# Kernel optimization log

Hardware: AMD Instinct MI355X
Metric: run time of the kernel (lower is better)

## Reference

```python
import jax, jax.numpy as jnp
import numpy as np

NUM_HEADS = 12


def setup_inputs() -> dict:
    key = jax.random.key(0)
    k1, k2, k3 = jax.random.split(key, 3)
    B, N, D = 8, 1024, 768
    x = jax.random.normal(k1, (B, N, D), dtype=jnp.float32)
    Wqkv = jax.random.normal(k2, (D, 3 * D), dtype=jnp.float32) * (D ** -0.5)
    Wproj = jax.random.normal(k3, (D, D), dtype=jnp.float32) * (D ** -0.5)
    bproj = jnp.zeros((D,), dtype=jnp.float32)
    return {"x": x, "Wqkv": Wqkv, "Wproj": Wproj, "bproj": bproj}


def reference(x, Wqkv, Wproj, bproj):
    B, N, D = x.shape
    H = NUM_HEADS
    d = D // H
    scale = d ** -0.5
    qkv = x @ Wqkv  # [B, N, 3D]; qkv_bias=False
    # 'b n (qkv h d) -> qkv b h n d'
    qkv = qkv.reshape(B, N, 3, H, d)
    q = jnp.transpose(qkv[:, :, 0], (0, 2, 1, 3))  # [B, H, N, d]
    k = jnp.transpose(qkv[:, :, 1], (0, 2, 1, 3))
    v = jnp.transpose(qkv[:, :, 2], (0, 2, 1, 3))
    attn = jnp.einsum('bhnd,bhmd->bhnm', q, k) * scale  # [B, H, N, N]
    attn = jax.nn.softmax(attn, axis=-1)
    out = jnp.einsum('bhnm,bhmd->bhnd', attn, v)  # [B, H, N, d]
    out = jnp.transpose(out, (0, 2, 1, 3)).reshape(B, N, D)  # 'b h n d -> b n (h d)'
    return out @ Wproj + bproj
```

## Files before the change

### kernel.cpp

```cpp
#include <hip/hip_runtime.h>
#include <math.h>
#include <stdint.h>

namespace {

constexpr int Nseq = 1024;
constexpr int Dm = 768;
constexpr int threeD = 2304;
constexpr int Mrows = 8192;
constexpr int Hh = 12;
constexpr float kScaleLog2 = 0.18033688011112042f;

using bf16x8 = __attribute__((ext_vector_type(8))) short;
using f32x4 = __attribute__((ext_vector_type(4))) float;
using f32x16 = __attribute__((ext_vector_type(16))) float;
using us4 = __attribute__((ext_vector_type(4))) unsigned short;

__device__ __forceinline__ unsigned short f2bf(float f) {
  union { float f; uint32_t u; } v;
  v.f = f;
  uint32_t r = v.u + 0x7fffu + ((v.u >> 16) & 1u);
  return (unsigned short)(r >> 16);
}

__device__ __forceinline__ float fexp2(float x) {
#if __has_builtin(__builtin_amdgcn_exp2f)
  return __builtin_amdgcn_exp2f(x);
#else
  float r;
  asm("v_exp_f32 %0, %1\n\ts_nop 0" : "=v"(r) : "v"(x));
  return r;
#endif
}

__device__ __forceinline__ uint32_t cvtpk_bf16(float lo, float hi) {
  uint32_t r;
  asm("v_cvt_pk_bf16_f32 %0, %1, %2" : "=v"(r) : "v"(lo), "v"(hi));
  return r;
}

__device__ __forceinline__ void gload_lds16(const void* g, void* l) {
  __builtin_amdgcn_global_load_lds(
      (const __attribute__((address_space(1))) unsigned int*)(uintptr_t)g,
      (__attribute__((address_space(3))) unsigned int*)(uintptr_t)l, 16, 0, 0);
}

__global__ __launch_bounds__(256) void cast_f32_bf16(
    const float* __restrict__ in, unsigned short* __restrict__ outp, int n4) {
  int i = blockIdx.x * blockDim.x + threadIdx.x;
  if (i < n4) {
    float4 v = ((const float4*)in)[i];
    us4 u = {f2bf(v.x), f2bf(v.y), f2bf(v.z), f2bf(v.w)};
    ((us4*)outp)[i] = u;
  }
}

__global__ __launch_bounds__(256) void transpose_cast(
    const float* __restrict__ W, unsigned short* __restrict__ Wt, int K, int N) {
  __shared__ unsigned short tile[32][33];
  const int n0 = blockIdx.x * 32, k0 = blockIdx.y * 32;
  const int tx = threadIdx.x & 31, ty = threadIdx.x >> 5;
#pragma unroll
  for (int i = 0; i < 32; i += 8)
    tile[ty + i][tx] = f2bf(W[(size_t)(k0 + ty + i) * N + n0 + tx]);
  __syncthreads();
#pragma unroll
  for (int i = 0; i < 32; i += 8)
    Wt[(size_t)(n0 + ty + i) * K + k0 + tx] = tile[tx][ty + i];
}

template <int MODE, int NCOLS>
__global__ __launch_bounds__(512) void gemm8(
    const unsigned short* __restrict__ A, const unsigned short* __restrict__ Bt,
    void* __restrict__ C0, void* __restrict__ C1,
    const float* __restrict__ bias, int Kdim) {
  __shared__ unsigned short As[2][128 * 64];
  __shared__ unsigned short Bs[2][256 * 64];
  const int tid = threadIdx.x;
  const int wid = tid >> 6, lane = tid & 63;
  const int l15 = lane & 15, lg = lane >> 4;
  const int p = blockIdx.x;
  const int cpx = gridDim.x >> 3;
  const int l = (p & 7) * cpx + (p >> 3);
  const int row0 = (l / NCOLS) * 128, col0 = (l % NCOLS) * 256;
  const int wr = (wid >> 2) * 64, wc = (wid & 3) * 64;

  auto stageA = [&](int kt, int b, int r) {
    const int s = r * 512 + tid;
    const int row = s >> 3, c = s & 7;
    const int sc = c ^ (row & 7);
    gload_lds16(&A[(size_t)(row0 + row) * Kdim + kt * 64 + sc * 8],
                &As[b][(s & ~63) * 8]);
  };
  auto stageB = [&](int kt, int b, int r) {
    const int s = r * 512 + tid;
    const int row = s >> 3, c = s & 7;
    const int sc = c ^ (row & 7);
    gload_lds16(&Bt[(size_t)(col0 + row) * Kdim + kt * 64 + sc * 8],
                &Bs[b][(s & ~63) * 8]);
  };
  auto rdA = [&](int b, int m, int ks) {
    const int row = wr + m * 16 + l15;
    const int sc = (ks * 4 + lg) ^ (row & 7);
    return *(const bf16x8*)&As[b][(row * 8 + sc) * 8];
  };
  auto rdB = [&](int b, int n, int ks) {
    const int row = wc + n * 16 + l15;
    const int sc = (ks * 4 + lg) ^ (row & 7);
    return *(const bf16x8*)&Bs[b][(row * 8 + sc) * 8];
  };

  f32x4 acc[4][4] = {};
  stageA(0, 0, 0);
  stageA(0, 0, 1);
  stageB(0, 0, 0);
  stageB(0, 0, 1);
  stageB(0, 0, 2);
  stageB(0, 0, 3);
  asm volatile("s_waitcnt vmcnt(0)" ::: "memory");
  __builtin_amdgcn_s_barrier();

  const int NTK = Kdim / 64;
  for (int g = 0; g < NTK; ++g) {
    const int cur = g & 1;
    const int nb = cur ^ 1;
    const bool pf = (g + 1 < NTK);
    bf16x8 bfr[4][2], afr[2][2];
#pragma unroll
    for (int n = 0; n < 4; ++n)
#pragma unroll
      for (int ks = 0; ks < 2; ++ks) bfr[n][ks] = rdB(cur, n, ks);
#pragma unroll
    for (int m = 0; m < 2; ++m)
#pragma unroll
      for (int ks = 0; ks < 2; ++ks) afr[m][ks] = rdA(cur, m, ks);
    if (pf) {
      stageA(g + 1, nb, 0);
      stageA(g + 1, nb, 1);
      stageB(g + 1, nb, 0);
    }
    __builtin_amdgcn_s_barrier();
    asm volatile("s_waitcnt lgkmcnt(0)" ::: "memory");
    __builtin_amdgcn_sched_barrier(0);
    __builtin_amdgcn_s_setprio(1);
#pragma unroll
    for (int m = 0; m < 2; ++m)
#pragma unroll
      for (int n = 0; n < 4; ++n)
#pragma unroll
        for (int ks = 0; ks < 2; ++ks)
          acc[m][n] = __builtin_amdgcn_mfma_f32_16x16x32_bf16(
              afr[m][ks], bfr[n][ks], acc[m][n], 0, 0, 0);
    __builtin_amdgcn_s_setprio(0);
    __builtin_amdgcn_s_barrier();
#pragma unroll
    for (int m = 0; m < 2; ++m)
#pragma unroll
      for (int ks = 0; ks < 2; ++ks) afr[m][ks] = rdA(cur, m + 2, ks);
    if (pf) {
      stageB(g + 1, nb, 1);
      stageB(g + 1, nb, 2);
      stageB(g + 1, nb, 3);
    }
    __builtin_amdgcn_s_barrier();
    asm volatile("s_waitcnt lgkmcnt(0)" ::: "memory");
    __builtin_amdgcn_sched_barrier(0);
    __builtin_amdgcn_s_setprio(1);
#pragma unroll
    for (int m = 0; m < 2; ++m)
#pragma unroll
      for (int n = 0; n < 4; ++n)
#pragma unroll
        for (int ks = 0; ks < 2; ++ks)
          acc[m + 2][n] = __builtin_amdgcn_mfma_f32_16x16x32_bf16(
              afr[m][ks], bfr[n][ks], acc[m + 2][n], 0, 0, 0);
    __builtin_amdgcn_s_setprio(0);
    asm volatile("s_waitcnt vmcnt(0)" ::: "memory");
    __builtin_amdgcn_sched_barrier(0);
    __builtin_amdgcn_s_barrier();
  }

  if constexpr (MODE == 1) {
#pragma unroll
    for (int m = 0; m < 4; ++m)
#pragma unroll
      for (int n = 0; n < 4; ++n) {
        const int col = col0 + wc + n * 16 + l15;
#pragma unroll
        for (int rr = 0; rr < 4; ++rr)
          ((float*)C0)[(size_t)(row0 + wr + m * 16 + lg * 4 + rr) * Dm + col] =
              acc[m][n][rr] + bias[col];
      }
  } else {
    if (col0 < 1536) {
#pragma unroll
      for (int m = 0; m < 4; ++m)
#pragma unroll
        for (int n = 0; n < 4; ++n) {
          const int col = col0 + wc + n * 16 + l15;
          const float qs = (col < 768) ? kScaleLog2 : 1.f;
#pragma unroll
          for (int rr = 0; rr < 4; ++rr)
            ((unsigned short*)C0)[(size_t)(row0 + wr + m * 16 + lg * 4 + rr) *
                                      1536 + col] = f2bf(acc[m][n][rr] * qs);
        }
    } else {
#pragma unroll
      for (int m = 0; m < 4; ++m)
#pragma unroll
        for (int n = 0; n < 4; ++n) {
          const int c = col0 + wc + n * 16 + l15 - 1536;
          const int row = row0 + wr + m * 16 + lg * 4;
          const int bb = row >> 10, n0 = row & 1023;
          us4 pk = {f2bf(acc[m][n][0]), f2bf(acc[m][n][1]), f2bf(acc[m][n][2]),
                    f2bf(acc[m][n][3])};
          *(us4*)&((unsigned short*)C1)[((size_t)bb * 768 + c) * 1024 + n0] = pk;
        }
    }
  }
}

__global__ __launch_bounds__(256) void attn_mfma(
    const unsigned short* __restrict__ qkb, const unsigned short* __restrict__ vtb,
    unsigned short* __restrict__ outb) {
  constexpr int NT = Nseq / 64;
  __shared__ unsigned short Ks[2][64 * 64];
  __shared__ unsigned short Vs[2][64 * 64];
  const int tid = threadIdx.x;
  const int wid = tid >> 6, lane = tid & 63;
  const int l31 = lane & 31, hi = lane >> 5;
  const int p = blockIdx.x;
  const int l = (p & 7) * 96 + (p >> 3);
  const int qt = l & 7;
  const int hb = l >> 3;
  const int h = hb % Hh, b = hb / Hh;
  const size_t rb = (size_t)b * Nseq;
  const int hoff = h * 64;
  const size_t vbase = ((size_t)b * 768 + hoff) * 1024;

  const int qrow = qt * 128 + wid * 32 + l31;
  bf16x8 Qf[4];
#pragma unroll
  for (int ks = 0; ks < 4; ++ks)
    Qf[ks] = *(const bf16x8*)&qkb[(rb + qrow) * 1536 + hoff + ks * 16 + hi * 8];

  int strow[2], scol[2];
#pragma unroll
  for (int it = 0; it < 2; ++it) {
    const int ci = it * 256 + wid * 64 + lane;
    const int tr = ci >> 3, cc = ci & 7;
    strow[it] = tr;
    scol[it] = (cc ^ (tr & 7)) * 8;
  }

  auto stage = [&](int kt, int bufi) {
#pragma unroll
    for (int it = 0; it < 2; ++it) {
      const int ldsoff = (it * 256 + wid * 64) * 8;
      gload_lds16(&qkb[(rb + kt * 64 + strow[it]) * 1536 + 768 + hoff + scol[it]],
                  &Ks[bufi][ldsoff]);
      gload_lds16(&vtb[vbase + (size_t)strow[it] * 1024 + kt * 64 + scol[it]],
                  &Vs[bufi][ldsoff]);
    }
  };

  float l_run = 0.f;
  f32x16 o0 = {}, o1 = {};

  stage(0, 0);

  for (int kt = 0; kt < NT; ++kt) {
    const int bufi = kt & 1;
    if (kt + 1 < NT) {
      stage(kt + 1, bufi ^ 1);
      asm volatile("s_waitcnt vmcnt(4)" ::: "memory");
    } else {
      asm volatile("s_waitcnt vmcnt(0)" ::: "memory");
    }
    __builtin_amdgcn_s_barrier();
    const unsigned short* ksb = Ks[bufi];
    const unsigned short* vsb = Vs[bufi];
    f32x16 s0 = {}, s1 = {};
    __builtin_amdgcn_s_setprio(1);
#pragma unroll
    for (int ks = 0; ks < 4; ++ks) {
      const int c = 2 * ks + hi;
      {
        const int tr = l31;
        bf16x8 kf = *(const bf16x8*)&ksb[tr * 64 + ((c ^ (tr & 7)) * 8)];
        s0 = __builtin_amdgcn_mfma_f32_32x32x16_bf16(kf, Qf[ks], s0, 0, 0, 0);
      }
      {
        const int tr = l31 + 32;
        bf16x8 kf = *(const bf16x8*)&ksb[tr * 64 + ((c ^ (tr & 7)) * 8)];
        s1 = __builtin_amdgcn_mfma_f32_32x32x16_bf16(kf, Qf[ks], s1, 0, 0, 0);
      }
    }
    __builtin_amdgcn_s_setprio(0);
#pragma unroll
    for (int i = 0; i < 16; ++i) {
      s0[i] = fexp2(s0[i]);
      s1[i] = fexp2(s1[i]);
    }
    float a[8];
#pragma unroll
    for (int i = 0; i < 8; ++i)
      a[i] = (s0[i] + s0[i + 8]) + (s1[i] + s1[i + 8]);
#pragma unroll
    for (int st = 4; st >= 1; st >>= 1)
#pragma unroll
      for (int i = 0; i < st; ++i) a[i] += a[i + st];
    l_run += a[0];
    bf16x8 Pf[4];
#pragma unroll
    for (int ks = 0; ks < 4; ++ks) {
      const f32x16 sv = (ks >> 1) ? s1 : s0;
      const int e0 = 8 * (ks & 1);
      uint32_t pe01 = cvtpk_bf16(sv[e0 + 0], sv[e0 + 1]);
      uint32_t pe23 = cvtpk_bf16(sv[e0 + 2], sv[e0 + 3]);
      uint32_t po01 = cvtpk_bf16(sv[e0 + 4], sv[e0 + 5]);
      uint32_t po23 = cvtpk_bf16(sv[e0 + 6], sv[e0 + 7]);
      asm("v_permlane32_swap_b32 %0, %1" : "+v"(pe01), "+v"(po01));
      asm("v_permlane32_swap_b32 %0, %1" : "+v"(pe23), "+v"(po23));
      union {
        uint32_t w[4];
        bf16x8 v;
      } u;
      u.w[0] = pe01;
      u.w[1] = pe23;
      u.w[2] = po01;
      u.w[3] = po23;
      Pf[ks] = u.v;
    }
    __builtin_amdgcn_s_setprio(1);
#pragma unroll
    for (int ks = 0; ks < 4; ++ks) {
      const int c = 2 * ks + hi;
      {
        const int tr = l31;
        bf16x8 vf = *(const bf16x8*)&vsb[tr * 64 + ((c ^ (tr & 7)) * 8)];
        o0 = __builtin_amdgcn_mfma_f32_32x32x16_bf16(vf, Pf[ks], o0, 0, 0, 0);
      }
      {
        const int tr = l31 + 32;
        bf16x8 vf = *(const bf16x8*)&vsb[tr * 64 + ((c ^ (tr & 7)) * 8)];
        o1 = __builtin_amdgcn_mfma_f32_32x32x16_bf16(vf, Pf[ks], o1, 0, 0, 0);
      }
    }
    __builtin_amdgcn_s_setprio(0);
    asm volatile("s_waitcnt lgkmcnt(0)" ::: "memory");
    __builtin_amdgcn_sched_barrier(0);
    __builtin_amdgcn_s_barrier();
  }
  const float lsum = l_run + __shfl_xor(l_run, 32);
  const float linv = 1.f / lsum;
  const size_t obase = (size_t)(rb + qrow) * Dm + hoff;
#pragma unroll
  for (int g = 0; g < 4; ++g) {
    us4 a4 = {f2bf(o0[g * 4 + 0] * linv), f2bf(o0[g * 4 + 1] * linv),
              f2bf(o0[g * 4 + 2] * linv), f2bf(o0[g * 4 + 3] * linv)};
    *(us4*)&outb[obase + g * 8 + hi * 4] = a4;
    us4 b4 = {f2bf(o1[g * 4 + 0] * linv), f2bf(o1[g * 4 + 1] * linv),
              f2bf(o1[g * 4 + 2] * linv), f2bf(o1[g * 4 + 3] * linv)};
    *(us4*)&outb[obase + 32 + g * 8 + hi * 4] = b4;
  }
}

}

extern "C" void kernel_launch(void* const* d_in, const int* in_sizes, int n_in,
                              void* d_out, int out_size, void* d_ws,
                              size_t ws_size, hipStream_t stream) {
  (void)in_sizes;
  (void)n_in;
  (void)out_size;
  (void)ws_size;
  const float* x = (const float*)d_in[0];
  const float* Wqkv = (const float*)d_in[1];
  const float* Wproj = (const float*)d_in[2];
  const float* bproj = (const float*)d_in[3];
  float* out = (float*)d_out;

  char* w = (char*)d_ws;
  unsigned short* xb = (unsigned short*)w;
  w += (size_t)Mrows * Dm * 2;
  unsigned short* wqkvt = (unsigned short*)w;
  w += (size_t)threeD * Dm * 2;
  unsigned short* wprojt = (unsigned short*)w;
  w += (size_t)Dm * Dm * 2;
  unsigned short* qkb = (unsigned short*)w;
  w += (size_t)Mrows * 1536 * 2;
  unsigned short* vtb = (unsigned short*)w;
  w += (size_t)96 * 64 * 1024 * 2;
  unsigned short* attnb = (unsigned short*)w;

  cast_f32_bf16<<<(Mrows * Dm / 4 + 255) / 256, 256, 0, stream>>>(
      x, xb, Mrows * Dm / 4);
  transpose_cast<<<dim3(threeD / 32, Dm / 32), 256, 0, stream>>>(
      Wqkv, wqkvt, Dm, threeD);
  transpose_cast<<<dim3(Dm / 32, Dm / 32), 256, 0, stream>>>(Wproj, wprojt, Dm, Dm);
  gemm8<0, 9><<<dim3(576), 512, 0, stream>>>(xb, wqkvt, qkb, vtb, nullptr, Dm);
  attn_mfma<<<dim3(768), 256, 0, stream>>>(qkb, vtb, attnb);
  gemm8<1, 3><<<dim3(192), 512, 0, stream>>>(attnb, wprojt, out, nullptr, bproj,
                                             Dm);
}
```

Baseline: 125.1 us.

## Load K and V fragments directly from global memory into registers in attention

The attention kernel no longer stages K and V tiles through double-buffered LDS with async global-to-LDS loads and barriers. Each wave now reads its own K and V MFMA fragments straight from global memory into registers every tile. This removes LDS traffic, block barriers and the priority hints. In exchange, the four waves fetch the same K/V data redundantly, there is no explicit prefetch overlap, and the strided 16-byte global loads may leave the kernel latency-bound.

```diff
diff --git a/kernel.cpp b/kernel.cpp
--- a/kernel.cpp
+++ b/kernel.cpp
@@ -224,8 +224,6 @@
     const unsigned short* __restrict__ qkb, const unsigned short* __restrict__ vtb,
     unsigned short* __restrict__ outb) {
   constexpr int NT = Nseq / 64;
-  __shared__ unsigned short Ks[2][64 * 64];
-  __shared__ unsigned short Vs[2][64 * 64];
   const int tid = threadIdx.x;
   const int wid = tid >> 6, lane = tid & 63;
   const int l31 = lane & 31, hi = lane >> 5;
@@ -236,7 +234,6 @@
   const int h = hb % Hh, b = hb / Hh;
   const size_t rb = (size_t)b * Nseq;
   const int hoff = h * 64;
-  const size_t vbase = ((size_t)b * 768 + hoff) * 1024;
 
   const int qrow = qt * 128 + wid * 32 + l31;
   bf16x8 Qf[4];
@@ -244,59 +241,33 @@
   for (int ks = 0; ks < 4; ++ks)
     Qf[ks] = *(const bf16x8*)&qkb[(rb + qrow) * 1536 + hoff + ks * 16 + hi * 8];
 
-  int strow[2], scol[2];
-#pragma unroll
-  for (int it = 0; it < 2; ++it) {
-    const int ci = it * 256 + wid * 64 + lane;
-    const int tr = ci >> 3, cc = ci & 7;
-    strow[it] = tr;
-    scol[it] = (cc ^ (tr & 7)) * 8;
-  }
-
-  auto stage = [&](int kt, int bufi) {
-#pragma unroll
-    for (int it = 0; it < 2; ++it) {
-      const int ldsoff = (it * 256 + wid * 64) * 8;
-      gload_lds16(&qkb[(rb + kt * 64 + strow[it]) * 1536 + 768 + hoff + scol[it]],
-                  &Ks[bufi][ldsoff]);
-      gload_lds16(&vtb[vbase + (size_t)strow[it] * 1024 + kt * 64 + scol[it]],
-                  &Vs[bufi][ldsoff]);
-    }
-  };
+  const unsigned short* Kb = qkb + rb * 1536 + 768 + hoff;
+  const unsigned short* Vb = vtb + ((size_t)b * 768 + hoff) * 1024;
 
   float l_run = 0.f;
   f32x16 o0 = {}, o1 = {};
 
-  stage(0, 0);
-
   for (int kt = 0; kt < NT; ++kt) {
-    const int bufi = kt & 1;
-    if (kt + 1 < NT) {
-      stage(kt + 1, bufi ^ 1);
-      asm volatile("s_waitcnt vmcnt(4)" ::: "memory");
-    } else {
-      asm volatile("s_waitcnt vmcnt(0)" ::: "memory");
-    }
-    __builtin_amdgcn_s_barrier();
-    const unsigned short* ksb = Ks[bufi];
-    const unsigned short* vsb = Vs[bufi];
+    const int k0 = kt * 64;
+    bf16x8 vf0[4], vf1[4], kf0[4], kf1[4];
+#pragma unroll
+    for (int ks = 0; ks < 4; ++ks) {
+      const int co = (2 * ks + hi) * 8;
+      vf0[ks] = *(const bf16x8*)&Vb[(size_t)l31 * 1024 + k0 + co];
+      vf1[ks] = *(const bf16x8*)&Vb[(size_t)(l31 + 32) * 1024 + k0 + co];
+    }
+#pragma unroll
+    for (int ks = 0; ks < 4; ++ks) {
+      const int co = (2 * ks + hi) * 8;
+      kf0[ks] = *(const bf16x8*)&Kb[(size_t)(k0 + l31) * 1536 + co];
+      kf1[ks] = *(const bf16x8*)&Kb[(size_t)(k0 + l31 + 32) * 1536 + co];
+    }
     f32x16 s0 = {}, s1 = {};
-    __builtin_amdgcn_s_setprio(1);
-#pragma unroll
-    for (int ks = 0; ks < 4; ++ks) {
-      const int c = 2 * ks + hi;
-      {
-        const int tr = l31;
-        bf16x8 kf = *(const bf16x8*)&ksb[tr * 64 + ((c ^ (tr & 7)) * 8)];
-        s0 = __builtin_amdgcn_mfma_f32_32x32x16_bf16(kf, Qf[ks], s0, 0, 0, 0);
-      }
-      {
-        const int tr = l31 + 32;
-        bf16x8 kf = *(const bf16x8*)&ksb[tr * 64 + ((c ^ (tr & 7)) * 8)];
-        s1 = __builtin_amdgcn_mfma_f32_32x32x16_bf16(kf, Qf[ks], s1, 0, 0, 0);
-      }
-    }
-    __builtin_amdgcn_s_setprio(0);
+#pragma unroll
+    for (int ks = 0; ks < 4; ++ks) {
+      s0 = __builtin_amdgcn_mfma_f32_32x32x16_bf16(kf0[ks], Qf[ks], s0, 0, 0, 0);
+      s1 = __builtin_amdgcn_mfma_f32_32x32x16_bf16(kf1[ks], Qf[ks], s1, 0, 0, 0);
+    }
 #pragma unroll
     for (int i = 0; i < 16; ++i) {
       s0[i] = fexp2(s0[i]);
@@ -332,25 +303,11 @@
       u.w[3] = po23;
       Pf[ks] = u.v;
     }
-    __builtin_amdgcn_s_setprio(1);
-#pragma unroll
-    for (int ks = 0; ks < 4; ++ks) {
-      const int c = 2 * ks + hi;
-      {
-        const int tr = l31;
-        bf16x8 vf = *(const bf16x8*)&vsb[tr * 64 + ((c ^ (tr & 7)) * 8)];
-        o0 = __builtin_amdgcn_mfma_f32_32x32x16_bf16(vf, Pf[ks], o0, 0, 0, 0);
-      }
-      {
-        const int tr = l31 + 32;
-        bf16x8 vf = *(const bf16x8*)&vsb[tr * 64 + ((c ^ (tr & 7)) * 8)];
-        o1 = __builtin_amdgcn_mfma_f32_32x32x16_bf16(vf, Pf[ks], o1, 0, 0, 0);
-      }
-    }
-    __builtin_amdgcn_s_setprio(0);
-    asm volatile("s_waitcnt lgkmcnt(0)" ::: "memory");
-    __builtin_amdgcn_sched_barrier(0);
-    __builtin_amdgcn_s_barrier();
+#pragma unroll
+    for (int ks = 0; ks < 4; ++ks) {
+      o0 = __builtin_amdgcn_mfma_f32_32x32x16_bf16(vf0[ks], Pf[ks], o0, 0, 0, 0);
+      o1 = __builtin_amdgcn_mfma_f32_32x32x16_bf16(vf1[ks], Pf[ks], o1, 0, 0, 0);
+    }
   }
   const float lsum = l_run + __shfl_xor(l_run, 32);
   const float linv = 1.f / lsum;
```

Result: slower. 174.5 us (+39.5%).
